# Optimization experiments

Hardware: AMD Instinct MI355X
Metric: run time of the kernel (lower is better)

The kernel has to match this reference:

```python
import jax, jax.numpy as jnp
import numpy as np
import math

RADIUS = 0.2
NSAMPLE = 32
M = 8
EPS = 1e-6

def _normalize(v, axis):
    n = jnp.sqrt(jnp.sum(v * v, axis=axis, keepdims=True))
    return v / (n + EPS)

def _ball_query(xyz, new_xyz, fps_idx):
    # Emulates pointnet2 ball_query: first NSAMPLE in-radius indices in scan
    # order, padded with the first found index; rows with no hits stay 0.
    B, N, _ = xyz.shape
    d2 = jnp.sum((new_xyz[:, :, None, :] - xyz[:, None, :, :]) ** 2, axis=-1)  # (B,P,N)
    mask = d2 < RADIUS * RADIUS
    keys = jnp.where(mask, jnp.arange(N, dtype=jnp.int32)[None, None, :], N)
    neg_top, _ = jax.lax.top_k(-keys, NSAMPLE)
    sorted_idx = -neg_top  # ascending first NSAMPLE in-radius indices (or N pads)
    cnt = jnp.sum(mask, axis=-1, keepdims=True)
    first = jnp.where(cnt > 0, jnp.minimum(sorted_idx[..., :1], N - 1), 0)
    j = jnp.arange(NSAMPLE)[None, None, :]
    idx = jnp.where(j < cnt, sorted_idx, first).astype(jnp.int32)
    return jnp.concatenate([fps_idx[:, :, None].astype(jnp.int32), idx], axis=-1)  # (B,P,S+1)

def _group(features, idx):
    # features (B,C,N), idx (B,P,S) -> (B,C,P,S)
    return jax.vmap(lambda f, i: f[:, i])(features, idx)

def _project_one(p):
    # reference vector in plane orthogonal to normalized p; p (B,3,P,1)
    p = _normalize(p, 1)
    px, py, pz = p[:, 0], p[:, 1], p[:, 2]
    colin = jnp.abs(px) > 1.0 - 1e-3
    rx = jnp.where(colin, -py * px, 1.0 - px * px)
    ry = jnp.where(colin, 1.0 - py * py, -px * py)
    rz = jnp.where(colin, -py * pz, -px * pz)
    return _normalize(jnp.stack([rx, ry, rz], axis=1), 1)

def _rot_sort(p, pts):
    # sort pts (B,3,P,S) along S by clockwise angle of projection onto plane orthogonal to p
    p = _normalize(p, 1)
    ref = _project_one(p)
    vert = jnp.sum(p * pts, axis=1, keepdims=True) * p
    projs = _normalize(pts - vert, 1)
    refb = jnp.broadcast_to(ref, projs.shape)
    sinus = jnp.sum(jnp.cross(refb, projs, axis=1) * p, axis=1, keepdims=True)
    cosinus = jnp.sum(refb * projs, axis=1, keepdims=True)
    angles = jnp.arctan2(sinus, cosinus)  # (B,1,P,S)
    close = jnp.sum(projs * projs, axis=1, keepdims=True) < 1e-12
    rnd = (jax.random.uniform(jax.random.key(42), angles.shape) - 0.5) * (2.0 * math.pi)
    angles = jnp.where(close, rnd, angles)
    ind = jnp.argsort(angles, axis=-1)
    return jnp.take_along_axis(pts, jnp.broadcast_to(ind, pts.shape), axis=-1)

def _calc_invariance(center, rel):
    norm2 = jnp.sqrt(jnp.sum(rel * rel, axis=1, keepdims=True) + 1e-12)
    c = _normalize(center, 1)
    cosang = jnp.sum(c * rel, axis=1, keepdims=True) / norm2
    angle = jnp.arccos(jnp.clip(cosang, -1.0 + EPS, 1.0 - EPS))
    return jnp.concatenate([norm2, angle], axis=1)  # (B,2,P,S)

def _to_quat(xyz):
    dist = jnp.sqrt(jnp.sum(xyz * xyz, axis=1, keepdims=True))
    ori = xyz / (dist + EPS)
    theta = dist / RADIUS * (math.pi / 2.0)
    return jnp.concatenate([jnp.cos(theta), jnp.sin(theta) * ori], axis=1)  # (B,4,P,S)

def _forward(xyz, new_xyz, fps_idx):
    idx = _ball_query(xyz, new_xyz, fps_idx)                 # (B,P,S+1)
    grouped = _group(jnp.swapaxes(xyz, 1, 2), idx)           # (B,3,P,S+1)
    centers = jnp.swapaxes(new_xyz, 1, 2)[..., None]         # (B,3,P,1)
    grouped = _rot_sort(centers, grouped[..., 1:] - centers) # (B,3,P,S)
    inv = _calc_invariance(centers, grouped)                 # (B,2,P,S)
    q = _to_quat(grouped)                                    # (B,4,P,S)
    quats = jnp.stack([jnp.roll(q, -m, axis=-1) for m in range(M)], axis=2)  # (B,4,M,P,S)
    B, _, _, P, S = quats.shape
    quats = quats.reshape(B, 4 * M, P, S)
    return jnp.concatenate([inv, quats], axis=1)             # (B,34,P,S)

def setup_inputs() -> dict:
    key = jax.random.key(0)
    k1, k2 = jax.random.split(key)
    B, N, P = 4, 8192, 2048
    xyz = jax.random.uniform(k1, (B, N, 3), dtype=jnp.float32)
    fps_idx = jax.random.randint(k2, (B, P), 0, N, dtype=jnp.int32)
    new_xyz = jax.vmap(lambda x, i: x[i])(xyz, fps_idx)
    return {"xyz": xyz, "new_xyz": new_xyz, "fps_idx": fps_idx}

def reference(xyz, new_xyz, fps_idx):
    return _forward(xyz, new_xyz, fps_idx)
```

## Files before the change

kernel.cpp:

```cpp
#include <hip/hip_runtime.h>
#include <math.h>

constexpr int Bc  = 4;
constexpr int Nc  = 8192;
constexpr int Pc  = 2048;
constexpr int Sc  = 32;
constexpr int CHc = 34;

#define THREEFRY_PARTITIONABLE 1

#define FMUL __fmul_rn
#define FADD __fadd_rn
#define FSUB __fsub_rn

__device__ __forceinline__ unsigned tf_rotl(unsigned x, int r) {
  return (x << r) | (x >> (32 - r));
}

__device__ __forceinline__ void threefry2x32_k42(unsigned& x0, unsigned& x1) {
  const unsigned ks0 = 0u, ks1 = 42u, ks2 = 0u ^ 42u ^ 0x1BD11BDAu;
  x0 += ks0; x1 += ks1;
#define TF_ROUND(r) { x0 += x1; x1 = tf_rotl(x1, (r)); x1 ^= x0; }
  TF_ROUND(13) TF_ROUND(15) TF_ROUND(26) TF_ROUND(6)
  x0 += ks1; x1 += ks2 + 1u;
  TF_ROUND(17) TF_ROUND(29) TF_ROUND(16) TF_ROUND(24)
  x0 += ks2; x1 += ks0 + 2u;
  TF_ROUND(13) TF_ROUND(15) TF_ROUND(26) TF_ROUND(6)
  x0 += ks0; x1 += ks1 + 3u;
  TF_ROUND(17) TF_ROUND(29) TF_ROUND(16) TF_ROUND(24)
  x0 += ks1; x1 += ks2 + 4u;
  TF_ROUND(13) TF_ROUND(15) TF_ROUND(26) TF_ROUND(6)
  x0 += ks2; x1 += ks0 + 5u;
#undef TF_ROUND
}

__device__ __forceinline__ float jax_rnd_angle(unsigned n) {
#if THREEFRY_PARTITIONABLE
  unsigned x0 = 0u, x1 = n;
  threefry2x32_k42(x0, x1);
  unsigned bits = x0 ^ x1;
#else
  const unsigned half = (unsigned)(Bc * Pc * Sc) / 2u;
  unsigned x0, x1;
  bool second = (n >= half);
  if (second) { x0 = n - half; x1 = n; } else { x0 = n; x1 = n + half; }
  threefry2x32_k42(x0, x1);
  unsigned bits = second ? x1 : x0;
#endif
  float u = __uint_as_float((bits >> 9) | 0x3F800000u) - 1.0f;
  return FMUL(FSUB(u, 0.5f), (float)(2.0 * 3.141592653589793));
}

__device__ __forceinline__ float dot3rn(float ax, float ay, float az,
                                        float bx, float by, float bz) {
  return FADD(FADD(FMUL(ax, bx), FMUL(ay, by)), FMUL(az, bz));
}

__global__ __launch_bounds__(256)
void qgq_kernel(const float* __restrict__ xyz,
                const float* __restrict__ new_xyz,
                float* __restrict__ out)
{
  __shared__ int sIdx[Sc];
  __shared__ unsigned long long smask[4];

  const int tid  = threadIdx.x;
  const int wave = tid >> 6;
  const int lane = tid & 63;
  const int q    = blockIdx.x;
  const int b    = q >> 11;
  const int p    = q & 2047;

  const float* xb = xyz + (size_t)b * Nc * 3;
  const float cx = new_xyz[((size_t)b * Pc + p) * 3 + 0];
  const float cy = new_xyz[((size_t)b * Pc + p) * 3 + 1];
  const float cz = new_xyz[((size_t)b * Pc + p) * 3 + 2];

  const float R2 = (float)(0.2 * 0.2);
  int before = 0;
  for (int base = 0; base < Nc; base += 256) {
    const int i = base + tid;
    const float x = xb[i * 3 + 0];
    const float y = xb[i * 3 + 1];
    const float z = xb[i * 3 + 2];
    const float dx = FSUB(cx, x);
    const float dy = FSUB(cy, y);
    const float dz = FSUB(cz, z);
    const float d2 = FADD(FADD(FMUL(dx, dx), FMUL(dy, dy)), FMUL(dz, dz));
    const bool m = d2 < R2;
    const unsigned long long mask = __ballot(m);
    if (lane == 0) smask[wave] = mask;
    __syncthreads();
    const int c0 = (int)__popcll(smask[0]);
    const int c1 = (int)__popcll(smask[1]);
    const int c2 = (int)__popcll(smask[2]);
    const int c3 = (int)__popcll(smask[3]);
    if (m) {
      int pos = before + (int)__popcll(mask & ((1ull << lane) - 1ull));
      if (wave > 0) pos += c0;
      if (wave > 1) pos += c1;
      if (wave > 2) pos += c2;
      if (pos < Sc) sIdx[pos] = i;
    }
    before += c0 + c1 + c2 + c3;
    if (before >= Sc) break;
    __syncthreads();
  }
  __syncthreads();
  int cnt = (before > Sc) ? Sc : before;

  if (wave != 0) return;

  const int j  = lane & 31;
  const int gi = sIdx[(j < cnt) ? j : 0];

  const float ptx = xb[gi * 3 + 0];
  const float pty = xb[gi * 3 + 1];
  const float ptz = xb[gi * 3 + 2];
  const float relx = FSUB(ptx, cx);
  const float rely = FSUB(pty, cy);
  const float relz = FSUB(ptz, cz);

  const float n1  = __fsqrt_rn(dot3rn(cx, cy, cz, cx, cy, cz));
  const float id1 = FADD(n1, 1e-6f);
  const float p1x = __fdiv_rn(cx, id1);
  const float p1y = __fdiv_rn(cy, id1);
  const float p1z = __fdiv_rn(cz, id1);

  const float n2  = __fsqrt_rn(dot3rn(p1x, p1y, p1z, p1x, p1y, p1z));
  const float id2 = FADD(n2, 1e-6f);
  const float p2x = __fdiv_rn(p1x, id2);
  const float p2y = __fdiv_rn(p1y, id2);
  const float p2z = __fdiv_rn(p1z, id2);

  const bool colin = fabsf(p2x) > (float)(1.0 - 0.001);
  const float rxv = colin ? FMUL(-p2y, p2x) : FSUB(1.0f, FMUL(p2x, p2x));
  const float ryv = colin ? FSUB(1.0f, FMUL(p2y, p2y)) : FMUL(-p2x, p2y);
  const float rzv = colin ? FMUL(-p2y, p2z) : FMUL(-p2x, p2z);
  const float nr  = __fsqrt_rn(dot3rn(rxv, ryv, rzv, rxv, ryv, rzv));
  const float idr = FADD(nr, 1e-6f);
  const float refx = __fdiv_rn(rxv, idr);
  const float refy = __fdiv_rn(ryv, idr);
  const float refz = __fdiv_rn(rzv, idr);

  const float sdot = dot3rn(p1x, p1y, p1z, relx, rely, relz);
  const float wx = FSUB(relx, FMUL(sdot, p1x));
  const float wy = FSUB(rely, FMUL(sdot, p1y));
  const float wz = FSUB(relz, FMUL(sdot, p1z));
  const float nw  = __fsqrt_rn(dot3rn(wx, wy, wz, wx, wy, wz));
  const float idw = FADD(nw, 1e-6f);
  const float prx = __fdiv_rn(wx, idw);
  const float pry = __fdiv_rn(wy, idw);
  const float prz = __fdiv_rn(wz, idw);

  const float s2 = dot3rn(prx, pry, prz, prx, pry, prz);

  float angle;
  if (s2 < 1e-12f) {
    const unsigned n = ((unsigned)q << 5) | (unsigned)j;
    angle = jax_rnd_angle(n);
  } else {
    const float ccx = FSUB(FMUL(refy, prz), FMUL(refz, pry));
    const float ccy = FSUB(FMUL(refz, prx), FMUL(refx, prz));
    const float ccz = FSUB(FMUL(refx, pry), FMUL(refy, prx));
    const float sinus   = dot3rn(ccx, ccy, ccz, p1x, p1y, p1z);
    const float cosinus = dot3rn(refx, refy, refz, prx, pry, prz);
    angle = atan2f(sinus, cosinus);
  }

  const unsigned ab   = __float_as_uint(angle);
  const unsigned skey = (ab & 0x80000000u) ? ~ab : (ab | 0x80000000u);
  unsigned long long key = ((unsigned long long)skey << 32) | (unsigned)j;

  #pragma unroll
  for (int k = 2; k <= 32; k <<= 1) {
    #pragma unroll
    for (int jj = k >> 1; jj > 0; jj >>= 1) {
      const unsigned long long other = __shfl_xor(key, jj);
      const bool up      = ((lane & k) == 0);
      const bool lower   = ((lane & jj) == 0);
      const bool takeMin = (lower == up);
      const unsigned long long mn = (key < other) ? key : other;
      const unsigned long long mx = (key < other) ? other : key;
      key = takeMin ? mn : mx;
    }
  }
  const int oj = (int)(key & 31u);

  const float sx = __shfl(relx, oj);
  const float sy = __shfl(rely, oj);
  const float sz = __shfl(relz, oj);

  const float dotr  = sx * sx + sy * sy + sz * sz;
  const float norm2 = sqrtf(dotr + 1e-12f);
  float cosang = (p1x * sx + p1y * sy + p1z * sz) / norm2;
  const float CL = (float)(1.0 - 1e-6);
  cosang = fminf(fmaxf(cosang, -CL), CL);
  const float ainv = acosf(cosang);

  const float dist = sqrtf(dotr);
  const float invd = 1.0f / (dist + 1e-6f);
  const float oxv = sx * invd, oyv = sy * invd, ozv = sz * invd;
  const float theta = (dist / 0.2f) * (float)(3.141592653589793 / 2.0);
  float st, ct;
  sincosf(theta, &st, &ct);
  const float qw = ct, qx = st * oxv, qy = st * oyv, qz = st * ozv;

  const size_t chs   = (size_t)Pc * Sc;
  const size_t baseo = (size_t)b * CHc * chs + (size_t)p * Sc + (size_t)j;

  if (lane < 32) {
    out[baseo + 0 * chs] = norm2;
    out[baseo + 1 * chs] = ainv;
  }
  #pragma unroll
  for (int m = 0; m < 8; ++m) {
    const int src = (j + m) & 31;
    const float vw = __shfl(qw, src);
    const float vx = __shfl(qx, src);
    const float vy = __shfl(qy, src);
    const float vz = __shfl(qz, src);
    if (lane < 32) {
      out[baseo + (size_t)(2 + 0 * 8 + m) * chs] = vw;
      out[baseo + (size_t)(2 + 1 * 8 + m) * chs] = vx;
      out[baseo + (size_t)(2 + 2 * 8 + m) * chs] = vy;
      out[baseo + (size_t)(2 + 3 * 8 + m) * chs] = vz;
    }
  }
}

extern "C" void kernel_launch(void* const* d_in, const int* in_sizes, int n_in,
                              void* d_out, int out_size, void* d_ws, size_t ws_size,
                              hipStream_t stream) {
  const float* xyz     = (const float*)d_in[0];
  const float* new_xyz = (const float*)d_in[1];
  float* out = (float*)d_out;

  const int nq = Bc * Pc;
  dim3 grid(nq), block(256);
  hipLaunchKernelGGL(qgq_kernel, grid, block, 0, stream, xyz, new_xyz, out);
}
```

Measured before the change: 92.64 us.

## Batch ball-query scan into 2048-point tiles with one barrier per tile

The ball-query scan now loads 8 points per thread (2048 per block) before computing, ballots all 8 masks, and writes per-chunk counts into a double-buffered shared array. A single barrier per tile replaces the two barriers per 256-point step, and each wave computes its prefix offsets from the 32 counts. This cuts barrier count and exposes more memory-level parallelism. The cost is scanning more points than needed when the first 32 hits come early, plus extra register pressure.

```diff
diff --git a/kernel.cpp b/kernel.cpp
--- a/kernel.cpp
+++ b/kernel.cpp
@@ -62,7 +62,7 @@
                 float* __restrict__ out)
 {
   __shared__ int sIdx[Sc];
-  __shared__ unsigned long long smask[4];
+  __shared__ int sCnt[2][32];
 
   const int tid  = threadIdx.x;
   const int wave = tid >> 6;
@@ -78,33 +78,58 @@
 
   const float R2 = (float)(0.2 * 0.2);
   int before = 0;
-  for (int base = 0; base < Nc; base += 256) {
-    const int i = base + tid;
-    const float x = xb[i * 3 + 0];
-    const float y = xb[i * 3 + 1];
-    const float z = xb[i * 3 + 2];
-    const float dx = FSUB(cx, x);
-    const float dy = FSUB(cy, y);
-    const float dz = FSUB(cz, z);
-    const float d2 = FADD(FADD(FMUL(dx, dx), FMUL(dy, dy)), FMUL(dz, dz));
-    const bool m = d2 < R2;
-    const unsigned long long mask = __ballot(m);
-    if (lane == 0) smask[wave] = mask;
+  #pragma unroll 1
+  for (int tile = 0; tile < Nc / 2048; ++tile) {
+    const int base = tile * 2048;
+    const int par  = tile & 1;
+
+    float xs[8], ys[8], zs[8];
+    #pragma unroll
+    for (int k = 0; k < 8; ++k) {
+      const int i = base + k * 256 + tid;
+      xs[k] = xb[i * 3 + 0];
+      ys[k] = xb[i * 3 + 1];
+      zs[k] = xb[i * 3 + 2];
+    }
+
+    unsigned long long msk[8];
+    bool mm[8];
+    #pragma unroll
+    for (int k = 0; k < 8; ++k) {
+      const float dx = FSUB(cx, xs[k]);
+      const float dy = FSUB(cy, ys[k]);
+      const float dz = FSUB(cz, zs[k]);
+      const float d2 = FADD(FADD(FMUL(dx, dx), FMUL(dy, dy)), FMUL(dz, dz));
+      mm[k]  = d2 < R2;
+      msk[k] = __ballot(mm[k]);
+    }
+
+    if (lane == 0) {
+      #pragma unroll
+      for (int k = 0; k < 8; ++k)
+        sCnt[par][k * 4 + wave] = (int)__popcll(msk[k]);
+    }
     __syncthreads();
-    const int c0 = (int)__popcll(smask[0]);
-    const int c1 = (int)__popcll(smask[1]);
-    const int c2 = (int)__popcll(smask[2]);
-    const int c3 = (int)__popcll(smask[3]);
-    if (m) {
-      int pos = before + (int)__popcll(mask & ((1ull << lane) - 1ull));
-      if (wave > 0) pos += c0;
-      if (wave > 1) pos += c1;
-      if (wave > 2) pos += c2;
-      if (pos < Sc) sIdx[pos] = i;
-    }
-    before += c0 + c1 + c2 + c3;
+
+    int run = before;
+    int pfx[8];
+    #pragma unroll
+    for (int c = 0; c < 32; ++c) {
+      if ((c & 3) == wave) pfx[c >> 2] = run;
+      run += sCnt[par][c];
+    }
+
+    const unsigned long long below = (1ull << lane) - 1ull;
+    #pragma unroll
+    for (int k = 0; k < 8; ++k) {
+      if (mm[k]) {
+        const int pos = pfx[k] + (int)__popcll(msk[k] & below);
+        if (pos < Sc) sIdx[pos] = base + k * 256 + tid;
+      }
+    }
+
+    before = run;
     if (before >= Sc) break;
-    __syncthreads();
   }
   __syncthreads();
   int cnt = (before > Sc) ? Sc : before;
```

Result: faster. 89.12 us (-3.8%).
